# Kernel tuning notes

Hardware: AMD Instinct MI355X
Metric: run time of the kernel (lower is better)

## Reference

```python
import jax, jax.numpy as jnp
import numpy as np

B, T, D, H = 1, 2049, 1024, 16
HD = D // H                      # head_dim = 64
MAX_SEQ = 1025
L = 2 * MAX_SEQ - 1              # = T (required by the module's relative shift)

def setup_inputs() -> dict:
    key = jax.random.key(0)
    ks = jax.random.split(key, 12)
    s = 0.02
    return {
        'q': jax.random.normal(ks[0], (B, T, D), dtype=jnp.float32),
        'k': jax.random.normal(ks[1], (B, T, D), dtype=jnp.float32),
        'v': jax.random.normal(ks[2], (B, T, D), dtype=jnp.float32),
        'mask': jnp.tril(jnp.ones((1, 1, T, T), dtype=jnp.int32)),  # causal
        'Wq_w': jax.random.normal(ks[3], (D, D), dtype=jnp.float32) * s,
        'Wq_b': jnp.zeros((D,), dtype=jnp.float32),
        'Wk_w': jax.random.normal(ks[4], (D, D), dtype=jnp.float32) * s,
        'Wk_b': jnp.zeros((D,), dtype=jnp.float32),
        'Wv_w': jax.random.normal(ks[5], (D, D), dtype=jnp.float32) * s,
        'Wv_b': jnp.zeros((D,), dtype=jnp.float32),
        'Er': jax.random.normal(ks[6], (L, HD), dtype=jnp.float32),
        'Wo_w': jax.random.normal(ks[7], (D, D), dtype=jnp.float32) * s,
        'Wo_b': jnp.zeros((D,), dtype=jnp.float32),
    }

def reference(q, k, v, mask, Wq_w, Wq_b, Wk_w, Wk_b, Wv_w, Wv_b, Er, Wo_w, Wo_b):
    b, t, d = q.shape
    def proj(x, w, bias):
        # nn.Linear: x @ W^T + b ; then (B,T,H,HD) -> (B,H,T,HD)
        return (x @ w.T + bias).reshape(b, t, H, HD).transpose(0, 2, 1, 3)
    qh = proj(q, Wq_w, Wq_b)
    kh = proj(k, Wk_w, Wk_b)
    vh = proj(v, Wv_w, Wv_b)
    scores = jnp.einsum('bhtd,bhsd->bhts', qh, kh)          # (B,H,T,T)
    QEr = jnp.einsum('bhtd,ld->bhtl', qh, Er)               # (B,H,T,L) with L == T
    # _relative_shift: pad a zero row on seq dim then drop first row ->
    # row i becomes QEr row i+1, last row zeros (faithful to torch code)
    rel = jnp.concatenate([QEr[:, :, 1:, :], jnp.zeros_like(QEr[:, :, :1, :])], axis=2)
    scores = scores + rel
    scores = jnp.where(mask[:, :, :t, :t] == 0, -jnp.inf, scores)
    attn = jax.nn.softmax(scores / (HD ** 0.5), axis=-1)
    ctx = jnp.einsum('bhts,bhsd->bthd', attn, vh).reshape(b, t, d)
    return ctx @ Wo_w.T + Wo_b
```

## Files before the change

kernel.cpp:

```cpp
#include <hip/hip_runtime.h>
#include <hip/hip_bf16.h>
#include <math.h>

constexpr int T_SEQ = 2049;
constexpr int D_MODEL = 1024;
constexpr int N_HEAD = 16;
constexpr int HEAD_DIM = 64;
constexpr int VT_STRIDE = 2112;
constexpr int T1_ROWS = 1152;

typedef __attribute__((ext_vector_type(8))) short short8;
typedef __attribute__((ext_vector_type(4))) short short4v;
typedef __attribute__((ext_vector_type(4))) float floatx4;

__device__ inline void load_lds16(const void* g, void* l) {
  __builtin_amdgcn_global_load_lds(
      (const __attribute__((address_space(1))) unsigned int*)g,
      (__attribute__((address_space(3))) unsigned int*)l, 16, 0, 0);
}

__device__ inline short8 cvt8_bf16(const float* p) {
  float4 a = *(const float4*)p, b = *(const float4*)(p + 4);
  __hip_bfloat16 t[8] = {__float2bfloat16(a.x), __float2bfloat16(a.y),
                         __float2bfloat16(a.z), __float2bfloat16(a.w),
                         __float2bfloat16(b.x), __float2bfloat16(b.y),
                         __float2bfloat16(b.z), __float2bfloat16(b.w)};
  return *(const short8*)t;
}

__device__ inline float bf2f(__hip_bfloat16 x) { return __bfloat162float(x); }

__global__ __launch_bounds__(256) void cast_all(
    const float* __restrict__ q, const float* __restrict__ k,
    const float* __restrict__ v, const float* __restrict__ wq,
    const float* __restrict__ wk, const float* __restrict__ wv,
    const float* __restrict__ wo, __hip_bfloat16* __restrict__ qo,
    __hip_bfloat16* __restrict__ ko, __hip_bfloat16* __restrict__ vo,
    __hip_bfloat16* __restrict__ wqo, __hip_bfloat16* __restrict__ wko,
    __hip_bfloat16* __restrict__ wvo, __hip_bfloat16* __restrict__ woo) {
  const int z = blockIdx.y;
  const float* in;
  __hip_bfloat16* out;
  int n;
  switch (z) {
    case 0: in = q; out = qo; n = T_SEQ * D_MODEL; break;
    case 1: in = k; out = ko; n = T_SEQ * D_MODEL; break;
    case 2: in = v; out = vo; n = T_SEQ * D_MODEL; break;
    case 3: in = wq; out = wqo; n = D_MODEL * D_MODEL; break;
    case 4: in = wk; out = wko; n = D_MODEL * D_MODEL; break;
    case 5: in = wv; out = wvo; n = D_MODEL * D_MODEL; break;
    default: in = wo; out = woo; n = D_MODEL * D_MODEL; break;
  }
  const int i = (blockIdx.x * 256 + threadIdx.x) * 8;
  if (i + 8 > n) return;
  *(short8*)(out + i) = cvt8_bf16(in + i);
}

template <int BN, int OUTK>
__global__ __launch_bounds__(256) void mfma_gemm(
    const __hip_bfloat16* __restrict__ A0, const __hip_bfloat16* __restrict__ A1,
    const __hip_bfloat16* __restrict__ A2, const __hip_bfloat16* __restrict__ W0,
    const __hip_bfloat16* __restrict__ W1, const __hip_bfloat16* __restrict__ W2,
    const float* __restrict__ bias0, const float* __restrict__ bias1,
    const float* __restrict__ bias2, void* C0, void* C1, void* C2, int M) {
  constexpr int K = D_MODEL;
  constexpr int NT = BN / 32;
  __shared__ __align__(16) __hip_bfloat16 As[128 * 64];
  __shared__ __align__(16) __hip_bfloat16 Bs[BN * 64];

  const int z = blockIdx.z;
  const short* A = (const short*)(z == 0 ? A0 : z == 1 ? A1 : A2);
  const short* W = (const short*)(z == 0 ? W0 : z == 1 ? W1 : W2);
  const float* bias = z == 0 ? bias0 : z == 1 ? bias1 : bias2;
  void* C = z == 0 ? C0 : z == 1 ? C1 : C2;

  const int tid = threadIdx.x;
  const int wave = tid >> 6, lane = tid & 63;
  const int col = lane & 15, quad = lane >> 4;
  const int wm = wave >> 1, wn = wave & 1;
  const int m0 = blockIdx.y * 128, n0 = blockIdx.x * BN;

  const int srow = lane >> 3;
  const int sslot = lane & 7;
  const int sch = sslot ^ srow;

  floatx4 acc[4][NT];
#pragma unroll
  for (int i = 0; i < 4; i++)
#pragma unroll
    for (int j = 0; j < NT; j++) acc[i][j] = (floatx4){0.f, 0.f, 0.f, 0.f};

  for (int k0 = 0; k0 < K; k0 += 64) {
    if (k0) __syncthreads();
#pragma unroll
    for (int i = 0; i < 4; i++) {
      const int rb = (wave * 4 + i) * 8;
      const int am = min(m0 + rb + srow, M - 1);
      load_lds16(A + (size_t)am * K + k0 + sch * 8, (char*)As + rb * 128);
    }
#pragma unroll
    for (int i = 0; i < BN / 32; i++) {
      const int rb = (wave * (BN / 32) + i) * 8;
      const int bn = n0 + rb + srow;
      load_lds16(W + (size_t)bn * K + k0 + sch * 8, (char*)Bs + rb * 128);
    }
    __syncthreads();

#pragma unroll
    for (int kk = 0; kk < 2; kk++) {
      short8 af[4], bf[NT];
#pragma unroll
      for (int t = 0; t < 4; t++) {
        const int ra = wm * 64 + t * 16 + col;
        af[t] = *(const short8*)(As + ra * 64 + ((kk * 4 + quad) ^ (ra & 7)) * 8);
      }
#pragma unroll
      for (int t = 0; t < NT; t++) {
        const int rb = wn * (BN / 2) + t * 16 + col;
        bf[t] = *(const short8*)(Bs + rb * 64 + ((kk * 4 + quad) ^ (rb & 7)) * 8);
      }
#pragma unroll
      for (int mt = 0; mt < 4; mt++)
#pragma unroll
        for (int nt = 0; nt < NT; nt++)
          acc[mt][nt] = __builtin_amdgcn_mfma_f32_16x16x32_bf16(af[mt], bf[nt],
                                                                acc[mt][nt], 0, 0, 0);
    }
  }

#pragma unroll
  for (int mt = 0; mt < 4; mt++) {
#pragma unroll
    for (int r = 0; r < 4; r++) {
      const int m = m0 + wm * 64 + mt * 16 + quad * 4 + r;
      if (m >= M) continue;
#pragma unroll
      for (int nt = 0; nt < NT; nt++) {
        const int n = n0 + wn * (BN / 2) + nt * 16 + col;
        const float val = acc[mt][nt][r] + bias[n];
        if (OUTK == 0) {
          ((float*)C)[(size_t)m * D_MODEL + n] = val;
        } else {
          if (z < 2) {
            const int h = n >> 6, hd = n & 63;
            ((__hip_bfloat16*)C)[((size_t)h * T_SEQ + m) * HEAD_DIM + hd] =
                __float2bfloat16(val);
          } else {
            ((__hip_bfloat16*)C)[(size_t)m * D_MODEL + n] = __float2bfloat16(val);
          }
        }
      }
    }
  }
}

__global__ __launch_bounds__(256) void transpose_v_er(
    const __hip_bfloat16* __restrict__ vpr, __hip_bfloat16* __restrict__ vt,
    const float* __restrict__ Er, __hip_bfloat16* __restrict__ er_bf) {
  const int tid = threadIdx.x;
  if (blockIdx.y == 16) {
    const int i = (blockIdx.x * 256 + tid) * 8;
    if (i + 8 <= T_SEQ * HEAD_DIM) *(short8*)(er_bf + i) = cvt8_bf16(Er + i);
    return;
  }
  if (blockIdx.x >= 33) return;

  __shared__ __align__(16) __hip_bfloat16 tile[64][72];
  const int t0 = blockIdx.x * 64;
  const int h = blockIdx.y;
  const short* plane = (const short*)vpr;
  short* oplane = (short*)(vt + (size_t)h * HEAD_DIM * VT_STRIDE);

  for (int idx = tid; idx < 64 * 8; idx += 256) {
    const int row = idx >> 3, ch = idx & 7;
    const int t = t0 + row;
    short8 v = {0, 0, 0, 0, 0, 0, 0, 0};
    if (t < T_SEQ) v = *(const short8*)(plane + (size_t)t * D_MODEL + h * 64 + ch * 8);
    *(short8*)&tile[row][ch * 8] = v;
  }
  __syncthreads();
  for (int idx = tid; idx < 64 * 8; idx += 256) {
    const int d = idx >> 3, ch = idx & 7;
    short8 v;
#pragma unroll
    for (int i = 0; i < 8; i++) v[i] = *(const short*)&tile[ch * 8 + i][d];
    *(short8*)(oplane + (size_t)d * VT_STRIDE + t0 + ch * 8) = v;
  }
}

__global__ __launch_bounds__(512, 4) void flash_attn(
    const __hip_bfloat16* __restrict__ qh, const __hip_bfloat16* __restrict__ kh,
    const __hip_bfloat16* __restrict__ er, const __hip_bfloat16* __restrict__ vt,
    __hip_bfloat16* __restrict__ ctx, __hip_bfloat16* __restrict__ O0,
    __hip_bfloat16* __restrict__ O1, float* __restrict__ l0g,
    float* __restrict__ l1g) {
  __shared__ __align__(16) __hip_bfloat16 Ks[2][64 * 128];
  __shared__ __align__(16) __hip_bfloat16 Vs[2][64 * 64];
  __shared__ __align__(16) __hip_bfloat16 Ps[8][1024];

  const int tid = threadIdx.x;
  const int h = blockIdx.y;
  const int b = blockIdx.x;

  const int qt = (b < 8) ? b : 8 + ((b - 8) >> 1);
  const int tq0 = qt * 128;
  const int jmax = min(tq0 + 127, T_SEQ - 1) >> 6;
  int j0, j1;
  bool alt;
  if (b < 8) {
    j0 = 0; j1 = jmax; alt = false;
  } else {
    const int mid = (jmax + 1) >> 1;
    alt = (b - 8) & 1;
    j0 = alt ? mid : 0;
    j1 = alt ? jmax : mid - 1;
  }

  const int wave = tid >> 6;
  const int lane = tid & 63;
  const int col = lane & 15;
  const int quad = lane >> 4;

  const short* qplane = (const short*)(qh + (size_t)h * T_SEQ * HEAD_DIM);
  const short* kplane = (const short*)(kh + (size_t)h * T_SEQ * HEAD_DIM);
  const short* eplane = (const short*)er;
  const short* vplane = (const short*)(vt + (size_t)h * HEAD_DIM * VT_STRIDE);

  const int t_abs = tq0 + wave * 16 + col;
  const int tload = min(t_abs, T_SEQ - 1);
  const bool hiz = (t_abs >= T_SEQ - 1);
  short8 aq[4];
#pragma unroll
  for (int kc = 0; kc < 4; kc++) {
    short8 v = *(const short8*)(qplane + (size_t)tload * 64 + kc * 32 + quad * 8);
    if (kc >= 2 && hiz) v = (short8){0, 0, 0, 0, 0, 0, 0, 0};
    aq[kc] = v;
  }

  floatx4 o[4];
  float l_lane = 0.f;
#pragma unroll
  for (int i = 0; i < 4; i++) o[i] = (floatx4){0.f, 0.f, 0.f, 0.f};

  const int tstrip = tq0 + wave * 16;
  __hip_bfloat16* psw = &Ps[wave][0];

#define STAGE_TILE(JJ, BUF)                                                        \
  {                                                                                \
    const int s0_ = (JJ) * 64;                                                     \
    _Pragma("unroll") for (int ii = 0; ii < 2; ii++) {                             \
      const int i_ = wave * 2 + ii;                                                \
      const int r_ = i_ * 4 + (lane >> 4);                                         \
      const int sl_ = lane & 15;                                                   \
      const int g_ = (sl_ & 8) | ((sl_ ^ (r_ & 7)) & 7);                           \
      const int s_ = min(s0_ + r_, T_SEQ - 1);                                     \
      const short* src_ = (g_ < 8) ? (kplane + (size_t)s_ * 64 + g_ * 8)           \
                                   : (eplane + (size_t)s_ * 64 + (g_ - 8) * 8);    \
      load_lds16(src_, (char*)&Ks[BUF][0] + i_ * 1024);                            \
    }                                                                              \
    {                                                                              \
      const int d_ = wave * 8 + (lane >> 3);                                       \
      const int sl_ = lane & 7;                                                    \
      const int g_ = sl_ ^ (d_ & 7);                                               \
      load_lds16(vplane + (size_t)d_ * VT_STRIDE + s0_ + g_ * 8,                   \
                 (char*)&Vs[BUF][0] + wave * 1024);                                \
    }                                                                              \
  }

  STAGE_TILE(j0, 0)
  int buf = 0;

  for (int j = j0; j <= j1; ++j, buf ^= 1) {
    __syncthreads();
    if (j < j1) STAGE_TILE(j + 1, buf ^ 1)

    const int s0 = j * 64;
    if (s0 > tstrip + 15) continue;

    const __hip_bfloat16* ks = &Ks[buf][0];
    const __hip_bfloat16* vs = &Vs[buf][0];

    floatx4 sacc[4];
#pragma unroll
    for (int st = 0; st < 4; st++) {
      floatx4 c = {0.f, 0.f, 0.f, 0.f};
      const int row = st * 16 + col;
#pragma unroll
      for (int kc = 0; kc < 4; kc++) {
        const int ch = kc * 4 + quad;
        const int slot = (ch & 8) | ((ch ^ (row & 7)) & 7);
        short8 ka = *(const short8*)(ks + row * 128 + slot * 8);
        c = __builtin_amdgcn_mfma_f32_16x16x32_bf16(ka, aq[kc], c, 0, 0, 0);
      }
      sacc[st] = c;
    }

    if (s0 + 63 > tstrip) {
#pragma unroll
      for (int st = 0; st < 4; st++) {
        const int sbase = s0 + st * 16 + quad * 4;
#pragma unroll
        for (int r = 0; r < 4; r++)
          if (sbase + r > t_abs) sacc[st][r] = -INFINITY;
      }
    }

    float rs = 0.f;
#pragma unroll
    for (int st = 0; st < 4; st++)
#pragma unroll
      for (int r = 0; r < 4; r++) {
        const float p = __expf(sacc[st][r] * 0.125f);
        sacc[st][r] = p;
        rs += p;
      }
    l_lane += rs;

#pragma unroll
    for (int st = 0; st < 4; st++) {
      __hip_bfloat16 pb[4];
#pragma unroll
      for (int r = 0; r < 4; r++) pb[r] = __float2bfloat16(sacc[st][r]);
      const int kcA = st >> 1;
      const int quadA = (st & 1) * 2 + (quad >> 1);
      const int off = ((kcA * 4 + quadA) * 16 + col) * 8 + (quad & 1) * 4;
      *(short4v*)(psw + off) = *(const short4v*)pb;
    }
    short8 pa[2];
#pragma unroll
    for (int kc = 0; kc < 2; kc++)
      pa[kc] = *(const short8*)(psw + ((kc * 4 + quad) * 16 + col) * 8);

#pragma unroll
    for (int nt = 0; nt < 4; nt++) {
      const int row = nt * 16 + col;
#pragma unroll
      for (int kc = 0; kc < 2; kc++) {
        const int slot = (kc * 4 + quad) ^ (row & 7);
        short8 vb = *(const short8*)(vs + row * 64 + slot * 8);
        o[nt] = __builtin_amdgcn_mfma_f32_16x16x32_bf16(pa[kc], vb, o[nt], 0, 0, 0);
      }
    }
  }

  l_lane += __shfl_xor(l_lane, 16, 64);
  l_lane += __shfl_xor(l_lane, 32, 64);

  if (b < 8) {
    const float linv = 1.0f / l_lane;
    float linv_r[4];
#pragma unroll
    for (int r = 0; r < 4; r++) linv_r[r] = __shfl(linv, quad * 4 + r, 64);
#pragma unroll
    for (int r = 0; r < 4; r++) {
      const int t = tstrip + quad * 4 + r;
#pragma unroll
      for (int nt = 0; nt < 4; nt++)
        ctx[(size_t)t * D_MODEL + h * 64 + nt * 16 + col] =
            __float2bfloat16(o[nt][r] * linv_r[r]);
    }
  } else {
    if (lane < 16) {
      const int t = tstrip + lane;
      if (t < T_SEQ) {
        if (!alt)
          l0g[h * T1_ROWS + (t - 1024)] = l_lane;
        else
          l1g[h * T1_ROWS + (t - 1024)] = l_lane;
      }
    }
#pragma unroll
    for (int r = 0; r < 4; r++) {
      const int t = tstrip + quad * 4 + r;
      if (t < T_SEQ) {
        __hip_bfloat16* dst = (!alt ? O0 : O1) + (size_t)(t - 1024) * D_MODEL;
#pragma unroll
        for (int nt = 0; nt < 4; nt++)
          dst[h * 64 + nt * 16 + col] = __float2bfloat16(o[nt][r]);
      }
    }
  }
}

__global__ __launch_bounds__(256) void finalize(
    const __hip_bfloat16* __restrict__ O0, const __hip_bfloat16* __restrict__ O1,
    const float* __restrict__ l0g, const float* __restrict__ l1g,
    __hip_bfloat16* __restrict__ ctx) {
  const int idx = blockIdx.x * 256 + threadIdx.x;
  const int tr = idx >> 7;
  const int t = 1024 + tr;
  if (t >= T_SEQ) return;
  const int ch = idx & 127;
  const int h = ch >> 3;

  const float l = l0g[h * T1_ROWS + tr] + l1g[h * T1_ROWS + tr];
  const __hip_bfloat16* a = O0 + (size_t)tr * D_MODEL + ch * 8;
  const __hip_bfloat16* bsrc = O1 + (size_t)tr * D_MODEL + ch * 8;
  const float inv = 1.0f / l;
  __hip_bfloat16 outv[8];
#pragma unroll
  for (int i = 0; i < 8; i++)
    outv[i] = __float2bfloat16((bf2f(a[i]) + bf2f(bsrc[i])) * inv);
  *(short8*)(ctx + (size_t)t * D_MODEL + ch * 8) = *(const short8*)outv;
}

extern "C" void kernel_launch(void* const* d_in, const int* in_sizes, int n_in,
                              void* d_out, int out_size, void* d_ws, size_t ws_size,
                              hipStream_t stream) {
  const float* q = (const float*)d_in[0];
  const float* k = (const float*)d_in[1];
  const float* v = (const float*)d_in[2];
  const float* Wq_w = (const float*)d_in[4];
  const float* Wq_b = (const float*)d_in[5];
  const float* Wk_w = (const float*)d_in[6];
  const float* Wk_b = (const float*)d_in[7];
  const float* Wv_w = (const float*)d_in[8];
  const float* Wv_b = (const float*)d_in[9];
  const float* Er = (const float*)d_in[10];
  const float* Wo_w = (const float*)d_in[11];
  const float* Wo_b = (const float*)d_in[12];
  float* out = (float*)d_out;

  char* ws = (char*)d_ws;
  const size_t sz_plane = (size_t)T_SEQ * D_MODEL * 2;
  const size_t sz_w = (size_t)D_MODEL * D_MODEL * 2;
  __hip_bfloat16* qbf = (__hip_bfloat16*)ws;
  __hip_bfloat16* kbf = (__hip_bfloat16*)(ws + sz_plane);
  __hip_bfloat16* vbf = (__hip_bfloat16*)(ws + 2 * sz_plane);
  char* wbase = ws + 3 * sz_plane;
  __hip_bfloat16* wob = (__hip_bfloat16*)(wbase);
  __hip_bfloat16* wqb = (__hip_bfloat16*)(wbase + sz_w);
  __hip_bfloat16* wkb = (__hip_bfloat16*)(wbase + 2 * sz_w);
  __hip_bfloat16* wvb = (__hip_bfloat16*)(wbase + 3 * sz_w);
  char* pbase = wbase + 4 * sz_w;
  __hip_bfloat16* qpr = (__hip_bfloat16*)(pbase);
  __hip_bfloat16* kpr = (__hip_bfloat16*)(pbase + sz_plane);
  __hip_bfloat16* vpr = (__hip_bfloat16*)(pbase + 2 * sz_plane);

  const size_t sz_vt = (size_t)N_HEAD * HEAD_DIM * VT_STRIDE * 2;
  const size_t sz_er = (size_t)T_SEQ * HEAD_DIM * 2;
  const size_t sz_Op = (size_t)T1_ROWS * D_MODEL * 2;
  const size_t sz_l = (size_t)N_HEAD * T1_ROWS * 4;
  __hip_bfloat16* vt = (__hip_bfloat16*)ws;
  __hip_bfloat16* er_bf = (__hip_bfloat16*)(ws + sz_vt);
  __hip_bfloat16* O0 = (__hip_bfloat16*)(ws + sz_vt + sz_er);
  __hip_bfloat16* O1 = (__hip_bfloat16*)(ws + sz_vt + sz_er + sz_Op);
  float* l0g = (float*)(ws + sz_vt + sz_er + 2 * sz_Op);
  float* l1g = (float*)(ws + sz_vt + sz_er + 2 * sz_Op + sz_l);
  __hip_bfloat16* ctxb = (__hip_bfloat16*)(wbase + sz_w);

  const dim3 blk(256);

  cast_all<<<dim3(1025, 7), blk, 0, stream>>>(q, k, v, Wq_w, Wk_w, Wv_w, Wo_w, qbf,
                                              kbf, vbf, wqb, wkb, wvb, wob);

  mfma_gemm<128, 2><<<dim3(8, 17, 3), blk, 0, stream>>>(
      qbf, kbf, vbf, wqb, wkb, wvb, Wq_b, Wk_b, Wv_b, qpr, kpr, vpr, T_SEQ);

  transpose_v_er<<<dim3(65, 17), blk, 0, stream>>>(vpr, vt, Er, er_bf);

  flash_attn<<<dim3(26, N_HEAD), dim3(512), 0, stream>>>(qpr, kpr, er_bf, vt, ctxb,
                                                         O0, O1, l0g, l1g);

  finalize<<<dim3((1025 * 128 + 255) / 256), blk, 0, stream>>>(O0, O1, l0g, l1g, ctxb);

  mfma_gemm<64, 0><<<dim3(16, 17, 1), blk, 0, stream>>>(
      ctxb, ctxb, ctxb, wob, wob, wob, Wo_b, Wo_b, Wo_b, out, out, out, T_SEQ);
}
```

Measured before the change: 203.2 us.

## Fuse V transpose into QKV GEMM, double-buffer GEMM, reorder attention blocks

```diff
diff --git a/kernel.cpp b/kernel.cpp
--- a/kernel.cpp
+++ b/kernel.cpp
@@ -34,10 +34,10 @@
     const float* __restrict__ q, const float* __restrict__ k,
     const float* __restrict__ v, const float* __restrict__ wq,
     const float* __restrict__ wk, const float* __restrict__ wv,
-    const float* __restrict__ wo, __hip_bfloat16* __restrict__ qo,
+    const float* __restrict__ er, __hip_bfloat16* __restrict__ qo,
     __hip_bfloat16* __restrict__ ko, __hip_bfloat16* __restrict__ vo,
     __hip_bfloat16* __restrict__ wqo, __hip_bfloat16* __restrict__ wko,
-    __hip_bfloat16* __restrict__ wvo, __hip_bfloat16* __restrict__ woo) {
+    __hip_bfloat16* __restrict__ wvo, __hip_bfloat16* __restrict__ ero) {
   const int z = blockIdx.y;
   const float* in;
   __hip_bfloat16* out;
@@ -49,7 +49,7 @@
     case 3: in = wq; out = wqo; n = D_MODEL * D_MODEL; break;
     case 4: in = wk; out = wko; n = D_MODEL * D_MODEL; break;
     case 5: in = wv; out = wvo; n = D_MODEL * D_MODEL; break;
-    default: in = wo; out = woo; n = D_MODEL * D_MODEL; break;
+    default: in = er; out = ero; n = T_SEQ * HEAD_DIM; break;
   }
   const int i = (blockIdx.x * 256 + threadIdx.x) * 8;
   if (i + 8 > n) return;
@@ -64,9 +64,14 @@
     const float* __restrict__ bias0, const float* __restrict__ bias1,
     const float* __restrict__ bias2, void* C0, void* C1, void* C2, int M) {
   constexpr int K = D_MODEL;
+  constexpr int BK = 32;
   constexpr int NT = BN / 32;
-  __shared__ __align__(16) __hip_bfloat16 As[128 * 64];
-  __shared__ __align__(16) __hip_bfloat16 Bs[BN * 64];
+  constexpr int AINST = 2;
+  constexpr int BINST = BN / 64;
+  constexpr int NLOADS = AINST + BINST;
+  __shared__ __align__(16) char smem[128 * 64 * 2 + BN * 64 * 2];
+  __hip_bfloat16* As = (__hip_bfloat16*)smem;
+  __hip_bfloat16* Bs = (__hip_bfloat16*)(smem + 128 * 64 * 2);
 
   const int z = blockIdx.z;
   const short* A = (const short*)(z == 0 ? A0 : z == 1 ? A1 : A2);
@@ -80,9 +85,8 @@
   const int wm = wave >> 1, wn = wave & 1;
   const int m0 = blockIdx.y * 128, n0 = blockIdx.x * BN;
 
-  const int srow = lane >> 3;
-  const int sslot = lane & 7;
-  const int sch = sslot ^ srow;
+  const int srow = lane >> 2;
+  const int sslot = lane & 3;
 
   floatx4 acc[4][NT];
 #pragma unroll
@@ -90,42 +94,93 @@
 #pragma unroll
     for (int j = 0; j < NT; j++) acc[i][j] = (floatx4){0.f, 0.f, 0.f, 0.f};
 
-  for (int k0 = 0; k0 < K; k0 += 64) {
-    if (k0) __syncthreads();
-#pragma unroll
-    for (int i = 0; i < 4; i++) {
-      const int rb = (wave * 4 + i) * 8;
-      const int am = min(m0 + rb + srow, M - 1);
-      load_lds16(A + (size_t)am * K + k0 + sch * 8, (char*)As + rb * 128);
-    }
-#pragma unroll
-    for (int i = 0; i < BN / 32; i++) {
-      const int rb = (wave * (BN / 32) + i) * 8;
-      const int bn = n0 + rb + srow;
-      load_lds16(W + (size_t)bn * K + k0 + sch * 8, (char*)Bs + rb * 128);
+#define STAGE_G(K0, BUF)                                                      \
+  {                                                                           \
+    _Pragma("unroll") for (int i = 0; i < AINST; i++) {                       \
+      const int r_ = (wave * AINST + i) * 16 + srow;                          \
+      const int ch = sslot ^ ((r_ >> 1) & 3);                                 \
+      const int am = min(m0 + r_, M - 1);                                     \
+      load_lds16(A + (size_t)am * K + (K0) + ch * 8,                          \
+                 (char*)As + (BUF)*8192 + (wave * AINST + i) * 1024);         \
+    }                                                                         \
+    _Pragma("unroll") for (int i = 0; i < BINST; i++) {                       \
+      const int r_ = (wave * BINST + i) * 16 + srow;                          \
+      const int ch = sslot ^ ((r_ >> 1) & 3);                                 \
+      load_lds16(W + (size_t)(n0 + r_) * K + (K0) + ch * 8,                   \
+                 (char*)Bs + (BUF) * (BN * 64) + (wave * BINST + i) * 1024);  \
+    }                                                                         \
+  }
+
+  STAGE_G(0, 0)
+
+  int buf = 0;
+  for (int k0 = 0; k0 < K; k0 += BK, buf ^= 1) {
+    if (k0 + BK < K) {
+      STAGE_G(k0 + BK, buf ^ 1)
+      asm volatile("s_waitcnt vmcnt(%0)" ::"i"(NLOADS) : "memory");
+    } else {
+      asm volatile("s_waitcnt vmcnt(0)" ::: "memory");
+    }
+    __builtin_amdgcn_s_barrier();
+
+    const __hip_bfloat16* as = As + buf * 4096;
+    const __hip_bfloat16* bs = Bs + buf * (BN * 32);
+    short8 af[4], bfr[NT];
+#pragma unroll
+    for (int t = 0; t < 4; t++) {
+      const int ra = wm * 64 + t * 16 + col;
+      af[t] = *(const short8*)(as + ra * 32 + ((quad ^ ((ra >> 1) & 3)) * 8));
+    }
+#pragma unroll
+    for (int t = 0; t < NT; t++) {
+      const int rb = wn * (BN / 2) + t * 16 + col;
+      bfr[t] = *(const short8*)(bs + rb * 32 + ((quad ^ ((rb >> 1) & 3)) * 8));
+    }
+#pragma unroll
+    for (int mt = 0; mt < 4; mt++)
+#pragma unroll
+      for (int nt = 0; nt < NT; nt++)
+        acc[mt][nt] = __builtin_amdgcn_mfma_f32_16x16x32_bf16(af[mt], bfr[nt],
+                                                              acc[mt][nt], 0, 0, 0);
+    asm volatile("" ::: "memory");
+    __builtin_amdgcn_s_barrier();
+  }
+#undef STAGE_G
+
+  if (OUTK == 2 && z == 2) {
+    short* Tt = (short*)smem;
+#pragma unroll
+    for (int mt = 0; mt < 4; mt++) {
+      const int mb = wm * 16 + mt * 4 + quad;
+#pragma unroll
+      for (int nt = 0; nt < NT; nt++) {
+        const int n = wn * (BN / 2) + nt * 16 + col;
+        const float bb = bias[n0 + n];
+        __hip_bfloat16 pk[4];
+#pragma unroll
+        for (int r = 0; r < 4; r++) pk[r] = __float2bfloat16(acc[mt][nt][r] + bb);
+        *(short4v*)((char*)Tt + n * 256 + ((mb ^ (n & 15)) << 3)) =
+            *(const short4v*)pk;
+      }
     }
     __syncthreads();
-
-#pragma unroll
-    for (int kk = 0; kk < 2; kk++) {
-      short8 af[4], bf[NT];
-#pragma unroll
-      for (int t = 0; t < 4; t++) {
-        const int ra = wm * 64 + t * 16 + col;
-        af[t] = *(const short8*)(As + ra * 64 + ((kk * 4 + quad) ^ (ra & 7)) * 8);
-      }
-#pragma unroll
-      for (int t = 0; t < NT; t++) {
-        const int rb = wn * (BN / 2) + t * 16 + col;
-        bf[t] = *(const short8*)(Bs + rb * 64 + ((kk * 4 + quad) ^ (rb & 7)) * 8);
-      }
-#pragma unroll
-      for (int mt = 0; mt < 4; mt++)
-#pragma unroll
-        for (int nt = 0; nt < NT; nt++)
-          acc[mt][nt] = __builtin_amdgcn_mfma_f32_16x16x32_bf16(af[mt], bf[nt],
-                                                                acc[mt][nt], 0, 0, 0);
-    }
+    const int n_loc = tid >> 1, half = tid & 1;
+    if (m0 + half * 64 < VT_STRIDE) {
+      const int ng = n0 + n_loc;
+      __hip_bfloat16* dst = (__hip_bfloat16*)C +
+                            ((size_t)(ng >> 6) * HEAD_DIM + (ng & 63)) * VT_STRIDE +
+                            m0 + half * 64;
+#pragma unroll
+      for (int c = 0; c < 8; c++) {
+        short4v lo = *(const short4v*)((char*)Tt + n_loc * 256 +
+                                       (((half * 16 + 2 * c) ^ (n_loc & 15)) << 3));
+        short4v hi = *(const short4v*)((char*)Tt + n_loc * 256 +
+                                       (((half * 16 + 2 * c + 1) ^ (n_loc & 15)) << 3));
+        short8 o8 = {lo[0], lo[1], lo[2], lo[3], hi[0], hi[1], hi[2], hi[3]};
+        *(short8*)((short*)dst + c * 8) = o8;
+      }
+    }
+    return;
   }
 
 #pragma unroll
@@ -141,50 +196,12 @@
         if (OUTK == 0) {
           ((float*)C)[(size_t)m * D_MODEL + n] = val;
         } else {
-          if (z < 2) {
-            const int h = n >> 6, hd = n & 63;
-            ((__hip_bfloat16*)C)[((size_t)h * T_SEQ + m) * HEAD_DIM + hd] =
-                __float2bfloat16(val);
-          } else {
-            ((__hip_bfloat16*)C)[(size_t)m * D_MODEL + n] = __float2bfloat16(val);
-          }
+          const int h = n >> 6, hd = n & 63;
+          ((__hip_bfloat16*)C)[((size_t)h * T_SEQ + m) * HEAD_DIM + hd] =
+              __float2bfloat16(val);
         }
       }
     }
-  }
-}
-
-__global__ __launch_bounds__(256) void transpose_v_er(
-    const __hip_bfloat16* __restrict__ vpr, __hip_bfloat16* __restrict__ vt,
-    const float* __restrict__ Er, __hip_bfloat16* __restrict__ er_bf) {
-  const int tid = threadIdx.x;
-  if (blockIdx.y == 16) {
-    const int i = (blockIdx.x * 256 + tid) * 8;
-    if (i + 8 <= T_SEQ * HEAD_DIM) *(short8*)(er_bf + i) = cvt8_bf16(Er + i);
-    return;
-  }
-  if (blockIdx.x >= 33) return;
-
-  __shared__ __align__(16) __hip_bfloat16 tile[64][72];
-  const int t0 = blockIdx.x * 64;
-  const int h = blockIdx.y;
-  const short* plane = (const short*)vpr;
-  short* oplane = (short*)(vt + (size_t)h * HEAD_DIM * VT_STRIDE);
-
-  for (int idx = tid; idx < 64 * 8; idx += 256) {
-    const int row = idx >> 3, ch = idx & 7;
-    const int t = t0 + row;
-    short8 v = {0, 0, 0, 0, 0, 0, 0, 0};
-    if (t < T_SEQ) v = *(const short8*)(plane + (size_t)t * D_MODEL + h * 64 + ch * 8);
-    *(short8*)&tile[row][ch * 8] = v;
-  }
-  __syncthreads();
-  for (int idx = tid; idx < 64 * 8; idx += 256) {
-    const int d = idx >> 3, ch = idx & 7;
-    short8 v;
-#pragma unroll
-    for (int i = 0; i < 8; i++) v[i] = *(const short*)&tile[ch * 8 + i][d];
-    *(short8*)(oplane + (size_t)d * VT_STRIDE + t0 + ch * 8) = v;
   }
 }
 
@@ -199,8 +216,10 @@
   __shared__ __align__(16) __hip_bfloat16 Ps[8][1024];
 
   const int tid = threadIdx.x;
-  const int h = blockIdx.y;
-  const int b = blockIdx.x;
+  const int id = blockIdx.x + 26 * blockIdx.y;
+  const int slot = id >> 3;
+  const int h = (id & 7) + 8 * (slot >= 26);
+  const int b = 25 - (slot >= 26 ? slot - 26 : slot);
 
   const int qt = (b < 8) ? b : 8 + ((b - 8) >> 1);
   const int tq0 = qt * 128;
@@ -281,6 +300,7 @@
     const __hip_bfloat16* vs = &Vs[buf][0];
 
     floatx4 sacc[4];
+    __builtin_amdgcn_s_setprio(1);
 #pragma unroll
     for (int st = 0; st < 4; st++) {
       floatx4 c = {0.f, 0.f, 0.f, 0.f};
@@ -288,12 +308,13 @@
 #pragma unroll
       for (int kc = 0; kc < 4; kc++) {
         const int ch = kc * 4 + quad;
-        const int slot = (ch & 8) | ((ch ^ (row & 7)) & 7);
-        short8 ka = *(const short8*)(ks + row * 128 + slot * 8);
+        const int slot2 = (ch & 8) | ((ch ^ (row & 7)) & 7);
+        short8 ka = *(const short8*)(ks + row * 128 + slot2 * 8);
         c = __builtin_amdgcn_mfma_f32_16x16x32_bf16(ka, aq[kc], c, 0, 0, 0);
       }
       sacc[st] = c;
     }
+    __builtin_amdgcn_s_setprio(0);
 
     if (s0 + 63 > tstrip) {
 #pragma unroll
@@ -331,16 +352,18 @@
     for (int kc = 0; kc < 2; kc++)
       pa[kc] = *(const short8*)(psw + ((kc * 4 + quad) * 16 + col) * 8);
 
+    __builtin_amdgcn_s_setprio(1);
 #pragma unroll
     for (int nt = 0; nt < 4; nt++) {
       const int row = nt * 16 + col;
 #pragma unroll
       for (int kc = 0; kc < 2; kc++) {
-        const int slot = (kc * 4 + quad) ^ (row & 7);
-        short8 vb = *(const short8*)(vs + row * 64 + slot * 8);
+        const int slot2 = (kc * 4 + quad) ^ (row & 7);
+        short8 vb = *(const short8*)(vs + row * 64 + slot2 * 8);
         o[nt] = __builtin_amdgcn_mfma_f32_16x16x32_bf16(pa[kc], vb, o[nt], 0, 0, 0);
       }
     }
+    __builtin_amdgcn_s_setprio(0);
   }
 
   l_lane += __shfl_xor(l_lane, 16, 64);
@@ -385,7 +408,13 @@
 __global__ __launch_bounds__(256) void finalize(
     const __hip_bfloat16* __restrict__ O0, const __hip_bfloat16* __restrict__ O1,
     const float* __restrict__ l0g, const float* __restrict__ l1g,
-    __hip_bfloat16* __restrict__ ctx) {
+    __hip_bfloat16* __restrict__ ctx, const float* __restrict__ wo_src,
+    __hip_bfloat16* __restrict__ wob) {
+  if (blockIdx.y == 1) {
+    const int i = (blockIdx.x * 256 + threadIdx.x) * 8;
+    if (i + 8 <= D_MODEL * D_MODEL) *(short8*)(wob + i) = cvt8_bf16(wo_src + i);
+    return;
+  }
   const int idx = blockIdx.x * 256 + threadIdx.x;
   const int tr = idx >> 7;
   const int t = 1024 + tr;
@@ -424,45 +453,43 @@
   char* ws = (char*)d_ws;
   const size_t sz_plane = (size_t)T_SEQ * D_MODEL * 2;
   const size_t sz_w = (size_t)D_MODEL * D_MODEL * 2;
-  __hip_bfloat16* qbf = (__hip_bfloat16*)ws;
-  __hip_bfloat16* kbf = (__hip_bfloat16*)(ws + sz_plane);
-  __hip_bfloat16* vbf = (__hip_bfloat16*)(ws + 2 * sz_plane);
-  char* wbase = ws + 3 * sz_plane;
-  __hip_bfloat16* wob = (__hip_bfloat16*)(wbase);
-  __hip_bfloat16* wqb = (__hip_bfloat16*)(wbase + sz_w);
-  __hip_bfloat16* wkb = (__hip_bfloat16*)(wbase + 2 * sz_w);
-  __hip_bfloat16* wvb = (__hip_bfloat16*)(wbase + 3 * sz_w);
-  char* pbase = wbase + 4 * sz_w;
-  __hip_bfloat16* qpr = (__hip_bfloat16*)(pbase);
-  __hip_bfloat16* kpr = (__hip_bfloat16*)(pbase + sz_plane);
-  __hip_bfloat16* vpr = (__hip_bfloat16*)(pbase + 2 * sz_plane);
-
   const size_t sz_vt = (size_t)N_HEAD * HEAD_DIM * VT_STRIDE * 2;
   const size_t sz_er = (size_t)T_SEQ * HEAD_DIM * 2;
   const size_t sz_Op = (size_t)T1_ROWS * D_MODEL * 2;
   const size_t sz_l = (size_t)N_HEAD * T1_ROWS * 4;
-  __hip_bfloat16* vt = (__hip_bfloat16*)ws;
-  __hip_bfloat16* er_bf = (__hip_bfloat16*)(ws + sz_vt);
-  __hip_bfloat16* O0 = (__hip_bfloat16*)(ws + sz_vt + sz_er);
-  __hip_bfloat16* O1 = (__hip_bfloat16*)(ws + sz_vt + sz_er + sz_Op);
-  float* l0g = (float*)(ws + sz_vt + sz_er + 2 * sz_Op);
-  float* l1g = (float*)(ws + sz_vt + sz_er + 2 * sz_Op + sz_l);
-  __hip_bfloat16* ctxb = (__hip_bfloat16*)(wbase + sz_w);
+
+  __hip_bfloat16* qbf = (__hip_bfloat16*)ws;
+  __hip_bfloat16* kbf = (__hip_bfloat16*)(ws + sz_plane);
+  __hip_bfloat16* vbf = (__hip_bfloat16*)(ws + 2 * sz_plane);
+  __hip_bfloat16* wqb = (__hip_bfloat16*)(ws + 3 * sz_plane);
+  __hip_bfloat16* wkb = (__hip_bfloat16*)(ws + 3 * sz_plane + sz_w);
+  __hip_bfloat16* wvb = (__hip_bfloat16*)(ws + 3 * sz_plane + 2 * sz_w);
+  char* hi = ws + 3 * sz_plane + 3 * sz_w;
+  __hip_bfloat16* qpr = (__hip_bfloat16*)hi;
+  __hip_bfloat16* kpr = (__hip_bfloat16*)(hi + sz_plane);
+  __hip_bfloat16* vt = (__hip_bfloat16*)(hi + 2 * sz_plane);
+  __hip_bfloat16* er_bf = (__hip_bfloat16*)(hi + 2 * sz_plane + sz_vt);
+
+  __hip_bfloat16* ctxb = (__hip_bfloat16*)ws;
+  __hip_bfloat16* O0 = (__hip_bfloat16*)(ws + sz_plane);
+  __hip_bfloat16* O1 = (__hip_bfloat16*)(ws + sz_plane + sz_Op);
+  float* l0g = (float*)(ws + sz_plane + 2 * sz_Op);
+  float* l1g = (float*)(ws + sz_plane + 2 * sz_Op + sz_l);
+  __hip_bfloat16* wob = (__hip_bfloat16*)(ws + 3 * sz_plane);
 
   const dim3 blk(256);
 
-  cast_all<<<dim3(1025, 7), blk, 0, stream>>>(q, k, v, Wq_w, Wk_w, Wv_w, Wo_w, qbf,
-                                              kbf, vbf, wqb, wkb, wvb, wob);
+  cast_all<<<dim3(1025, 7), blk, 0, stream>>>(q, k, v, Wq_w, Wk_w, Wv_w, Er, qbf,
+                                              kbf, vbf, wqb, wkb, wvb, er_bf);
 
   mfma_gemm<128, 2><<<dim3(8, 17, 3), blk, 0, stream>>>(
-      qbf, kbf, vbf, wqb, wkb, wvb, Wq_b, Wk_b, Wv_b, qpr, kpr, vpr, T_SEQ);
-
-  transpose_v_er<<<dim3(65, 17), blk, 0, stream>>>(vpr, vt, Er, er_bf);
+      qbf, kbf, vbf, wqb, wkb, wvb, Wq_b, Wk_b, Wv_b, qpr, kpr, vt, T_SEQ);
 
   flash_attn<<<dim3(26, N_HEAD), dim3(512), 0, stream>>>(qpr, kpr, er_bf, vt, ctxb,
                                                          O0, O1, l0g, l1g);
 
-  finalize<<<dim3((1025 * 128 + 255) / 256), blk, 0, stream>>>(O0, O1, l0g, l1g, ctxb);
+  finalize<<<dim3((1025 * 128 + 255) / 256, 2), blk, 0, stream>>>(
+      O0, O1, l0g, l1g, ctxb, Wo_w, wob);
 
   mfma_gemm<64, 0><<<dim3(16, 17, 1), blk, 0, stream>>>(
       ctxb, ctxb, ctxb, wob, wob, wob, Wo_b, Wo_b, Wo_b, out, out, out, T_SEQ);
```

New measurement: 192.6 us. 1.06x faster.
